# Optimization experiments

Measured on AMD Instinct MI355X. Metric: run time of the kernel, lower is better.

The kernel has to match this reference:

```python
import jax, jax.numpy as jnp
import numpy as np
import math

B, N, DIM, H, DH, NNULL = 2, 2048, 1024, 16, 64, 2
SCALE = 8.0
LN_EPS = 1e-5


def _alibi_slopes(heads):
    # heads is a power of 2 here (16): slopes = start * start**i
    start = 2.0 ** (-(2.0 ** (-(math.log2(heads) - 3))))
    return np.array([start * (start ** i) for i in range(heads)], dtype=np.float32)


def setup_inputs() -> dict:
    key = jax.random.key(0)
    ks = jax.random.split(key, 6)
    inner = H * DH
    return {
        "x": jax.random.normal(ks[0], (B, N, DIM), dtype=jnp.float32),
        "norm_g": jnp.ones((DIM,), jnp.float32),
        "norm_b": jnp.zeros((DIM,), jnp.float32),
        "Wq": jax.random.normal(ks[1], (DIM, inner), jnp.float32) * 0.02,
        "Wkv": jax.random.normal(ks[2], (DIM, 2 * inner), jnp.float32) * 0.02,
        "q_scale": jnp.ones((DH,), jnp.float32),
        "k_scale": jnp.ones((DH,), jnp.float32),
        "null_kv": jax.random.normal(ks[3], (H, 2 * NNULL, DH), jnp.float32),
        "Wout": jax.random.normal(ks[4], (inner, DIM), jnp.float32) * 0.02,
    }


def _l2norm(t):
    # matches F.normalize: x / max(||x||, 1e-12)
    n = jnp.sqrt(jnp.sum(t * t, axis=-1, keepdims=True))
    return t / jnp.maximum(n, 1e-12)


def reference(x, norm_g, norm_b, Wq, Wkv, q_scale, k_scale, null_kv, Wout):
    b, n, dim = x.shape
    h, dh, nn = H, DH, NNULL
    j = n + nn

    # NOTE: faithful to source -- K/V come from the PRE-norm x (kv_input bound
    # before x = self.norm(x)); only Q uses the LayerNorm'd x.
    mu = jnp.mean(x, axis=-1, keepdims=True)
    var = jnp.mean((x - mu) ** 2, axis=-1, keepdims=True)
    xn = (x - mu) * jax.lax.rsqrt(var + LN_EPS) * norm_g + norm_b

    q = (xn @ Wq).reshape(b, n, h, dh).transpose(0, 2, 1, 3)          # b h n d
    kv = x @ Wkv
    k, v = jnp.split(kv, 2, axis=-1)
    k = k.reshape(b, n, h, dh).transpose(0, 2, 1, 3)                   # b h n d
    v = v.reshape(b, n, h, dh).transpose(0, 2, 1, 3)

    # null kv: (h, 2*nn, dh) -> (h, nn, 2, dh)
    null = null_kv.reshape(h, nn, 2, dh)
    nk = jnp.broadcast_to(null[:, :, 0, :][None], (b, h, nn, dh))
    nv = jnp.broadcast_to(null[:, :, 1, :][None], (b, h, nn, dh))
    k = jnp.concatenate([nk, k], axis=2)                               # b h j d
    v = jnp.concatenate([nv, v], axis=2)

    q = _l2norm(q) * q_scale
    k = _l2norm(k) * k_scale

    sim = jnp.einsum('bhid,bhjd->bhij', q, k) * SCALE                  # b h n j

    # ALiBi bias: rows at positions j-n..j-1, cols 0..j-1
    irow = jnp.arange(j - n, j)
    jcol = jnp.arange(j)
    bias = -jnp.abs(jcol[None, :] - irow[:, None]).astype(sim.dtype)   # (n, j)
    slopes = jnp.asarray(_alibi_slopes(h))[:, None, None]              # (h,1,1)
    sim = sim + slopes * bias

    # causal mask: triu with offset j - n + 1 (null kv always visible)
    causal = jnp.triu(jnp.ones((n, j), dtype=bool), k=j - n + 1)
    neg = jnp.finfo(sim.dtype).max
    sim = jnp.where(causal[None, None], -neg, sim)

    attn = jax.nn.softmax(sim, axis=-1)
    out = jnp.einsum('bhij,bhjd->bhid', attn, v)
    out = out.transpose(0, 2, 1, 3).reshape(b, n, h * dh)
    return out @ Wout
```

## Files before the change

### kernel.cpp

```cpp
#include <hip/hip_runtime.h>
#include <stdint.h>

#define H_    16
#define N_    2048
#define DIM_  1024
#define DH_   64
#define NN_   2
#define J_    2050
#define JP_   2112
#define B_    2
#define M_    4096
#define NSEG_ 84

typedef unsigned short u16;
typedef unsigned int u32;
typedef short bf16x8 __attribute__((ext_vector_type(8)));
typedef float f32x4 __attribute__((ext_vector_type(4)));

__device__ __forceinline__ u16 f2b(float f) {
  union { float f; unsigned int i; } v; v.f = f;
  unsigned int r = v.i + 0x7fffu + ((v.i >> 16) & 1u);
  return (u16)(r >> 16);
}
__device__ __forceinline__ float b2f(u16 u) {
  union { unsigned int i; float f; } v; v.i = ((unsigned int)u) << 16; return v.f;
}
__device__ __forceinline__ float lo2f(u32 u) {
  union { u32 i; float f; } v; v.i = u << 16; return v.f;
}
__device__ __forceinline__ float hi2f(u32 u) {
  union { u32 i; float f; } v; v.i = u & 0xffff0000u; return v.f;
}
__device__ __forceinline__ void unp8(const uint4 u, float* d) {
  d[0] = lo2f(u.x); d[1] = hi2f(u.x); d[2] = lo2f(u.y); d[3] = hi2f(u.y);
  d[4] = lo2f(u.z); d[5] = hi2f(u.z); d[6] = lo2f(u.w); d[7] = hi2f(u.w);
}
__device__ __forceinline__ void dma16(const u16* g, u16* l) {
  __builtin_amdgcn_global_load_lds(
      (const __attribute__((address_space(1))) u32*)(const void*)g,
      (__attribute__((address_space(3))) u32*)(void*)l, 16, 0, 0);
}

__global__ __launch_bounds__(256) void ktranspose_cast(const float* __restrict__ in,
                                                       u16* __restrict__ out, int R, int C) {
  __shared__ float tile[32][33];
  int tx = threadIdx.x & 31, ty = threadIdx.x >> 5;
  int c0 = blockIdx.x * 32, r0 = blockIdx.y * 32;
  #pragma unroll
  for (int i = 0; i < 32; i += 8)
    tile[ty + i][tx] = in[(size_t)(r0 + ty + i) * C + c0 + tx];
  __syncthreads();
  #pragma unroll
  for (int i = 0; i < 32; i += 8)
    out[(size_t)(c0 + ty + i) * R + r0 + tx] = f2b(tile[tx][ty + i]);
}

__global__ __launch_bounds__(256) void lnorm_k(const float* __restrict__ x,
                                               const float* __restrict__ g,
                                               const float* __restrict__ bb,
                                               u16* __restrict__ xn,
                                               u16* __restrict__ xbf) {
  int row = blockIdx.x;
  int t = threadIdx.x;
  float4 rw = *(const float4*)(x + (size_t)row * DIM_ + t * 4);
  float v0 = rw.x, v1 = rw.y, v2 = rw.z, v3 = rw.w;
  uint2 cw;
  cw.x = (unsigned)f2b(v0) | ((unsigned)f2b(v1) << 16);
  cw.y = (unsigned)f2b(v2) | ((unsigned)f2b(v3) << 16);
  *(uint2*)(xbf + (size_t)row * DIM_ + t * 4) = cw;
  float s = v0 + v1 + v2 + v3;
  float ss = v0 * v0 + v1 * v1 + v2 * v2 + v3 * v3;
  #pragma unroll
  for (int o = 32; o; o >>= 1) { s += __shfl_xor(s, o, 64); ss += __shfl_xor(ss, o, 64); }
  __shared__ float red[8];
  int lane = t & 63, w = t >> 6;
  if (lane == 0) { red[w] = s; red[4 + w] = ss; }
  __syncthreads();
  float S = red[0] + red[1] + red[2] + red[3];
  float SS = red[4] + red[5] + red[6] + red[7];
  float mu = S * (1.0f / DIM_);
  float var = SS * (1.0f / DIM_) - mu * mu;
  float rs = rsqrtf(var + 1e-5f);
  float4 gv = *(const float4*)(g + t * 4);
  float4 bv = *(const float4*)(bb + t * 4);
  uint2 ow;
  ow.x = (unsigned)f2b((v0 - mu) * rs * gv.x + bv.x) |
         ((unsigned)f2b((v1 - mu) * rs * gv.y + bv.y) << 16);
  ow.y = (unsigned)f2b((v2 - mu) * rs * gv.z + bv.z) |
         ((unsigned)f2b((v3 - mu) * rs * gv.w + bv.w) << 16);
  *(uint2*)(xn + (size_t)row * DIM_ + t * 4) = ow;
}

template <int MODE>
__global__ __launch_bounds__(256, 4) void gemm_k(const u16* __restrict__ A,
                                                 const u16* __restrict__ BT,
                                                 void* __restrict__ dst0,
                                                 void* __restrict__ dst1,
                                                 const float* __restrict__ scale,
                                                 int M, int Nc, int K) {
  __shared__ u16 As[128 * 32];
  __shared__ u16 Bs[64 * 32];
  int tid = threadIdx.x, wv = tid >> 6, lane = tid & 63;
  int fm = lane & 15, fg = lane >> 4;
  int row0 = blockIdx.y * 128, col0 = blockIdx.x * 64;
  f32x4 acc[2][4] = {};
  int lr = lane >> 2, lc8 = (lane & 3) * 8;
  const u16* Ag = A + (size_t)(row0 + wv * 32 + lr) * K + lc8;
  const u16* Bg = BT + (size_t)(col0 + wv * 16 + lr) * K + lc8;
  u16* AsW = As + wv * 1024;
  u16* BsW = Bs + wv * 512;
  for (int k0 = 0; k0 < K; k0 += 32) {
    __syncthreads();
    dma16(Ag + k0, AsW);
    dma16(Ag + (size_t)16 * K + k0, AsW + 512);
    dma16(Bg + k0, BsW);
    __syncthreads();
    bf16x8 af0 = *(const bf16x8*)&As[(wv * 32 + fm) * 32 + fg * 8];
    bf16x8 af1 = *(const bf16x8*)&As[(wv * 32 + 16 + fm) * 32 + fg * 8];
    #pragma unroll
    for (int nt = 0; nt < 4; nt++) {
      bf16x8 bfr = *(const bf16x8*)&Bs[(nt * 16 + fm) * 32 + fg * 8];
      acc[0][nt] = __builtin_amdgcn_mfma_f32_16x16x32_bf16(af0, bfr, acc[0][nt], 0, 0, 0);
      acc[1][nt] = __builtin_amdgcn_mfma_f32_16x16x32_bf16(af1, bfr, acc[1][nt], 0, 0, 0);
    }
  }
  if (MODE == 1) {
    float* C = (float*)dst0;
    #pragma unroll
    for (int mt = 0; mt < 2; mt++)
      #pragma unroll
      for (int nt = 0; nt < 4; nt++)
        #pragma unroll
        for (int r = 0; r < 4; r++) {
          int m = row0 + wv * 32 + mt * 16 + fg * 4 + r;
          C[(size_t)m * Nc + col0 + nt * 16 + fm] = acc[mt][nt][r];
        }
  } else {
    bool isK = (MODE == 2) || (col0 < 1024);
    int h = ((MODE == 2) ? col0 : (isK ? col0 : col0 - 1024)) >> 6;
    float sv[4];
    if (isK) {
      #pragma unroll
      for (int nt = 0; nt < 4; nt++) sv[nt] = scale[nt * 16 + fm];
    }
    u16* Do = (u16*)((MODE == 3 && !isK) ? dst1 : dst0);
    #pragma unroll
    for (int mt = 0; mt < 2; mt++) {
      #pragma unroll
      for (int r = 0; r < 4; r++) {
        float inv = 1.0f;
        if (isK) {
          float ssp = 0.0f;
          #pragma unroll
          for (int nt = 0; nt < 4; nt++) ssp += acc[mt][nt][r] * acc[mt][nt][r];
          #pragma unroll
          for (int o = 1; o <= 8; o <<= 1) ssp += __shfl_xor(ssp, o, 64);
          inv = 1.0f / fmaxf(sqrtf(ssp), 1e-12f);
        }
        int m = row0 + wv * 32 + mt * 16 + fg * 4 + r;
        int b = m >> 11, n = m & 2047;
        size_t base;
        if (MODE == 2)      base = (((size_t)(b * H_ + h)) * N_ + n) * 64;
        else if (isK)       base = (((size_t)(b * H_ + h)) * JP_ + (n + NN_)) * 64;
        else                base = (((size_t)(b * H_ + h)) * J_ + (n + NN_)) * 64;
        #pragma unroll
        for (int nt = 0; nt < 4; nt++) {
          float val = acc[mt][nt][r];
          if (isK) val = val * inv * sv[nt];
          Do[base + nt * 16 + fm] = f2b(val);
        }
      }
    }
  }
}

__global__ __launch_bounds__(256) void vtransp_k(const u16* __restrict__ Vb,
                                                 const float* __restrict__ nkv,
                                                 const float* __restrict__ ks,
                                                 u16* __restrict__ Kb,
                                                 u16* __restrict__ VTp) {
  __shared__ u16 tile[64][80];
  int t = threadIdx.x;
  int c = blockIdx.x, bh = blockIdx.y, h = bh & 15;
  int jl = t >> 2, dc = (t & 3) * 16;
  int j = c * 64 + jl;
  if (j < NN_) {
    float kvv[16];
    float kssp = 0.0f;
    #pragma unroll
    for (int e = 0; e < 16; e++) {
      float vv = nkv[(size_t)(h * 4 + 2 * j + 1) * 64 + dc + e];
      tile[jl][dc + e] = f2b(vv);
      float kv = nkv[(size_t)(h * 4 + 2 * j) * 64 + dc + e];
      kvv[e] = kv; kssp += kv * kv;
    }
    kssp += __shfl_xor(kssp, 1, 64);
    kssp += __shfl_xor(kssp, 2, 64);
    float inv = 1.0f / fmaxf(sqrtf(kssp), 1e-12f);
    #pragma unroll
    for (int e = 0; e < 16; e++)
      Kb[((size_t)bh * JP_ + j) * 64 + dc + e] = f2b(kvv[e] * inv * ks[dc + e]);
  } else if (j < J_) {
    const uint4* src = (const uint4*)(Vb + ((size_t)bh * J_ + j) * 64 + dc);
    *(uint4*)&tile[jl][dc] = src[0];
    *(uint4*)&tile[jl][dc + 8] = src[1];
  } else {
    uint4 z = {0, 0, 0, 0};
    *(uint4*)&tile[jl][dc] = z;
    *(uint4*)&tile[jl][dc + 8] = z;
  }
  __syncthreads();
  int d = t >> 2, p0 = (t & 3) * 16;
  u16 tmp[16] __attribute__((aligned(16)));
  #pragma unroll
  for (int e = 0; e < 16; e++) {
    int pos = p0 + e;
    int h2 = pos >> 5, rem = pos & 31;
    int fgp = rem >> 3, tt = rem & 7;
    int nt = tt >> 2, r = tt & 3;
    int jloc = (h2 * 2 + nt) * 16 + fgp * 4 + r;
    tmp[e] = tile[jloc][d];
  }
  uint4* dstp = (uint4*)(VTp + ((size_t)bh * 64 + d) * JP_ + c * 64 + p0);
  dstp[0] = ((uint4*)tmp)[0];
  dstp[1] = ((uint4*)tmp)[1];
}

__global__ __launch_bounds__(256, 6) void attn_k(const u16* __restrict__ Qn,
                                                 const u16* __restrict__ Kb,
                                                 const u16* __restrict__ VTp,
                                                 const float* __restrict__ qs,
                                                 const float* __restrict__ ks,
                                                 u16* __restrict__ partials) {
  __shared__ u16 Ks0[64 * 32], Ks1[64 * 32];
  __shared__ u16 Vs0[64 * 32], Vs1[64 * 32];
  int tid = threadIdx.x;
  int wv = tid >> 6, lane = tid & 63;
  int fm = lane & 15, fg = lane >> 4;
  int bh = blockIdx.y, h = bh & 15;
  int cum = 0, qt = 0, seg = 0;
  #pragma unroll 1
  for (int i = 0; i < 32; i++) {
    int t = 31 - i, s = (t + 9) >> 3;
    if ((int)blockIdx.x < cum + s) { qt = t; seg = (int)blockIdx.x - cum; break; }
    cum += s;
  }
  int q0 = qt * 64;
  int q = q0 + wv * 16 + fm;
  float slope = exp2f(-0.5f * (float)(h + 1));
  float prod = fabsf(qs[lane] * ks[lane]);
  #pragma unroll
  for (int o = 32; o; o >>= 1) prod = fmaxf(prod, __shfl_xor(prod, o, 64));
  float Mb = 8.0f * prod;
  const u16* qp = Qn + ((size_t)bh * N_ + q) * 64 + fg * 8;
  bf16x8 qf0 = *(const bf16x8*)(qp);
  bf16x8 qf1 = *(const bf16x8*)(qp + 32);
  f32x4 accO[4] = {};
  float lp = 0.0f;
  int lr = lane >> 2, lc8 = (lane & 3) * 8;
  const u16* KbBH = Kb + (size_t)bh * JP_ * 64;
  const u16* VTbh = VTp + (size_t)bh * 64 * JP_;
  int c0 = seg * 8;
  int c1 = min(c0 + 8, qt + 2);
  for (int c = c0; c < c1; c++) {
    int jb = c * 64;
    __syncthreads();
    const u16* Kg = KbBH + (size_t)jb * 64 + (size_t)(wv * 16 + lr) * 64 + lc8;
    dma16(Kg,      Ks0 + wv * 512);
    dma16(Kg + 32, Ks1 + wv * 512);
    const u16* Vg = VTbh + (size_t)(wv * 16 + lr) * JP_ + jb + lc8;
    dma16(Vg,      Vs0 + wv * 512);
    dma16(Vg + 32, Vs1 + wv * 512);
    __syncthreads();
    f32x4 accS[4] = {};
    #pragma unroll
    for (int nt = 0; nt < 4; nt++) {
      bf16x8 kf0 = *(const bf16x8*)&Ks0[(nt * 16 + fm) * 32 + fg * 8];
      accS[nt] = __builtin_amdgcn_mfma_f32_16x16x32_bf16(kf0, qf0, accS[nt], 0, 0, 0);
      bf16x8 kf1 = *(const bf16x8*)&Ks1[(nt * 16 + fm) * 32 + fg * 8];
      accS[nt] = __builtin_amdgcn_mfma_f32_16x16x32_bf16(kf1, qf1, accS[nt], 0, 0, 0);
    }
    union { bf16x8 v; u16 s[8]; } P0, P1;
    #pragma unroll
    for (int nt = 0; nt < 4; nt++) {
      #pragma unroll
      for (int r = 0; r < 4; r++) {
        int jj = jb + nt * 16 + fg * 4 + r;
        float arg = fmaf(accS[nt][r], 8.0f, slope * (float)(jj - q - 2)) - Mb;
        float p = (jj <= q + 2) ? __expf(arg) : 0.0f;
        u16 pb = f2b(p);
        lp += b2f(pb);
        if (nt < 2) P0.s[nt * 4 + r] = pb;
        else        P1.s[(nt - 2) * 4 + r] = pb;
      }
    }
    #pragma unroll
    for (int nt = 0; nt < 4; nt++) {
      bf16x8 vf0 = *(const bf16x8*)&Vs0[(nt * 16 + fm) * 32 + fg * 8];
      accO[nt] = __builtin_amdgcn_mfma_f32_16x16x32_bf16(vf0, P0.v, accO[nt], 0, 0, 0);
      bf16x8 vf1 = *(const bf16x8*)&Vs1[(nt * 16 + fm) * 32 + fg * 8];
      accO[nt] = __builtin_amdgcn_mfma_f32_16x16x32_bf16(vf1, P1.v, accO[nt], 0, 0, 0);
    }
  }
  lp += __shfl_xor(lp, 16, 64);
  lp += __shfl_xor(lp, 32, 64);
  u16* P = partials + ((size_t)bh * NSEG_ + blockIdx.x) * 4224;
  int sq = wv * 16 + fm;
  #pragma unroll
  for (int nt = 0; nt < 4; nt++) {
    uint2 ow;
    ow.x = (unsigned)f2b(accO[nt][0]) | ((unsigned)f2b(accO[nt][1]) << 16);
    ow.y = (unsigned)f2b(accO[nt][2]) | ((unsigned)f2b(accO[nt][3]) << 16);
    *(uint2*)(P + sq * 64 + nt * 16 + fg * 4) = ow;
  }
  if (fg == 0) *(float*)(P + 4096 + 2 * sq) = lp;
}

__global__ __launch_bounds__(256) void comb_k(const u16* __restrict__ partials,
                                              u16* __restrict__ AO) {
  int qt = blockIdx.x, bh = blockIdx.y, b = bh >> 4, h = bh & 15;
  int t = threadIdx.x, q = t >> 2, dq = (t & 3) * 16;
  int s = (qt + 9) >> 3;
  int cum = 0;
  for (int tt = qt + 1; tt < 32; tt++) cum += (tt + 9) >> 3;
  float acc[16] = {};
  float lsum = 0.0f;
  for (int k = 0; k < s; k++) {
    const u16* P = partials + ((size_t)bh * NSEG_ + cum + k) * 4224;
    uint4 a = *(const uint4*)(P + q * 64 + dq);
    uint4 bq = *(const uint4*)(P + q * 64 + dq + 8);
    float tmp[8];
    unp8(a, tmp);
    #pragma unroll
    for (int e = 0; e < 8; e++) acc[e] += tmp[e];
    unp8(bq, tmp);
    #pragma unroll
    for (int e = 0; e < 8; e++) acc[8 + e] += tmp[e];
    lsum += *(const float*)(P + 4096 + 2 * q);
  }
  float linv = 1.0f / lsum;
  int n = qt * 64 + q;
  u16* dst = AO + (((size_t)(b * N_ + n)) * H_ + h) * 64 + dq;
  u16 ov[16] __attribute__((aligned(16)));
  #pragma unroll
  for (int e = 0; e < 16; e++) ov[e] = f2b(acc[e] * linv);
  *(uint4*)dst = ((uint4*)ov)[0];
  *(uint4*)(dst + 8) = ((uint4*)ov)[1];
}

extern "C" void kernel_launch(void* const* d_in, const int* in_sizes, int n_in,
                              void* d_out, int out_size, void* d_ws, size_t ws_size,
                              hipStream_t stream) {
  const float* x    = (const float*)d_in[0];
  const float* ng   = (const float*)d_in[1];
  const float* nb   = (const float*)d_in[2];
  const float* Wq   = (const float*)d_in[3];
  const float* Wkv  = (const float*)d_in[4];
  const float* qs   = (const float*)d_in[5];
  const float* ks   = (const float*)d_in[6];
  const float* nkv  = (const float*)d_in[7];
  const float* Wout = (const float*)d_in[8];
  float* out = (float*)d_out;
  char* ws = (char*)d_ws;

  u16* xn    = (u16*)(ws + 0);
  u16* WoutT = (u16*)(ws + 8388608);
  u16* Qn    = (u16*)(ws + 10485760);
  u16* Kb    = (u16*)(ws + 18874368);
  u16* VTp   = (u16*)(ws + 27525120);
  u16* xbf   = (u16*)(ws + 36175872);
  u16* WqT   = (u16*)(ws + 44564480);
  u16* WkvT  = (u16*)(ws + 46661632);
  u16* Vb    = (u16*)(ws + 50855936);
  u16* parts = xbf;
  u16* AO    = xn;

  hipMemsetAsync(Kb, 0, 8650752, stream);
  ktranspose_cast<<<dim3(32, 32), 256, 0, stream>>>(Wq, WqT, 1024, 1024);
  ktranspose_cast<<<dim3(64, 32), 256, 0, stream>>>(Wkv, WkvT, 1024, 2048);
  ktranspose_cast<<<dim3(32, 32), 256, 0, stream>>>(Wout, WoutT, 1024, 1024);
  lnorm_k<<<4096, 256, 0, stream>>>(x, ng, nb, xn, xbf);
  gemm_k<2><<<dim3(16, 32), 256, 0, stream>>>(xn, WqT, Qn, nullptr, qs, M_, 1024, 1024);
  gemm_k<3><<<dim3(32, 32), 256, 0, stream>>>(xbf, WkvT, Kb, Vb, ks, M_, 2048, 1024);
  vtransp_k<<<dim3(33, 32), 256, 0, stream>>>(Vb, nkv, ks, Kb, VTp);
  attn_k<<<dim3(NSEG_, 32), 256, 0, stream>>>(Qn, Kb, VTp, qs, ks, parts);
  comb_k<<<dim3(32, 32), 256, 0, stream>>>(parts, AO);
  gemm_k<1><<<dim3(16, 32), 256, 0, stream>>>(AO, WoutT, out, nullptr, nullptr, M_, 1024, 1024);
}
```

Measured before the change: 238.8 us.

## Enlarge GEMM tiles to 128x128, fold scale into Q, streamline attention softmax

The GEMM kernel moves from 128x64 to 128x128 block tiles, with each wave computing a 64x64 sub-tile from 4 A and 4 B fragments. This raises MFMA reuse per LDS read and halves the grid. The Q projection now folds the factor of 8 into the q scale. The attention softmax uses precomputed ALiBi offsets, a mask-free fast path for tiles that lie fully below the diagonal, and packed bf16 conversion intrinsics. The larger tile raises register pressure and drops the occupancy hint, and the max-offset term must still agree with the pre-scaled Q.

Result: slower. 286.2 us (+19.9%).

```diff
diff --git a/kernel.cpp b/kernel.cpp
--- a/kernel.cpp
+++ b/kernel.cpp
@@ -1,4 +1,5 @@
 #include <hip/hip_runtime.h>
+#include <hip/hip_bf16.h>
 #include <stdint.h>
 
 #define H_    16
@@ -35,6 +36,11 @@
   d[0] = lo2f(u.x); d[1] = hi2f(u.x); d[2] = lo2f(u.y); d[3] = hi2f(u.y);
   d[4] = lo2f(u.z); d[5] = hi2f(u.z); d[6] = lo2f(u.w); d[7] = hi2f(u.w);
 }
+__device__ __forceinline__ u32 pk2(float a, float b) {
+  union { __hip_bfloat162 h; u32 u; } x;
+  x.h = __float22bfloat162_rn(make_float2(a, b));
+  return x.u;
+}
 __device__ __forceinline__ void dma16(const u16* g, u16* l) {
   __builtin_amdgcn_global_load_lds(
       (const __attribute__((address_space(1))) u32*)(const void*)g,
@@ -65,8 +71,8 @@
   float4 rw = *(const float4*)(x + (size_t)row * DIM_ + t * 4);
   float v0 = rw.x, v1 = rw.y, v2 = rw.z, v3 = rw.w;
   uint2 cw;
-  cw.x = (unsigned)f2b(v0) | ((unsigned)f2b(v1) << 16);
-  cw.y = (unsigned)f2b(v2) | ((unsigned)f2b(v3) << 16);
+  cw.x = pk2(v0, v1);
+  cw.y = pk2(v2, v3);
   *(uint2*)(xbf + (size_t)row * DIM_ + t * 4) = cw;
   float s = v0 + v1 + v2 + v3;
   float ss = v0 * v0 + v1 * v1 + v2 * v2 + v3 * v3;
@@ -84,68 +90,74 @@
   float4 gv = *(const float4*)(g + t * 4);
   float4 bv = *(const float4*)(bb + t * 4);
   uint2 ow;
-  ow.x = (unsigned)f2b((v0 - mu) * rs * gv.x + bv.x) |
-         ((unsigned)f2b((v1 - mu) * rs * gv.y + bv.y) << 16);
-  ow.y = (unsigned)f2b((v2 - mu) * rs * gv.z + bv.z) |
-         ((unsigned)f2b((v3 - mu) * rs * gv.w + bv.w) << 16);
+  ow.x = pk2((v0 - mu) * rs * gv.x + bv.x, (v1 - mu) * rs * gv.y + bv.y);
+  ow.y = pk2((v2 - mu) * rs * gv.z + bv.z, (v3 - mu) * rs * gv.w + bv.w);
   *(uint2*)(xn + (size_t)row * DIM_ + t * 4) = ow;
 }
 
 template <int MODE>
-__global__ __launch_bounds__(256, 4) void gemm_k(const u16* __restrict__ A,
-                                                 const u16* __restrict__ BT,
-                                                 void* __restrict__ dst0,
-                                                 void* __restrict__ dst1,
-                                                 const float* __restrict__ scale,
-                                                 int M, int Nc, int K) {
+__global__ __launch_bounds__(256) void gemm_k(const u16* __restrict__ A,
+                                              const u16* __restrict__ BT,
+                                              void* __restrict__ dst0,
+                                              void* __restrict__ dst1,
+                                              const float* __restrict__ scale,
+                                              int M, int Nc, int K) {
   __shared__ u16 As[128 * 32];
-  __shared__ u16 Bs[64 * 32];
+  __shared__ u16 Bs[128 * 32];
   int tid = threadIdx.x, wv = tid >> 6, lane = tid & 63;
   int fm = lane & 15, fg = lane >> 4;
-  int row0 = blockIdx.y * 128, col0 = blockIdx.x * 64;
-  f32x4 acc[2][4] = {};
+  int row0 = blockIdx.y * 128, col0 = blockIdx.x * 128;
+  int wr = (wv & 1) * 64, wc = (wv >> 1) * 64;
+  f32x4 acc[4][4] = {};
   int lr = lane >> 2, lc8 = (lane & 3) * 8;
   const u16* Ag = A + (size_t)(row0 + wv * 32 + lr) * K + lc8;
-  const u16* Bg = BT + (size_t)(col0 + wv * 16 + lr) * K + lc8;
+  const u16* Bg = BT + (size_t)(col0 + wv * 32 + lr) * K + lc8;
   u16* AsW = As + wv * 1024;
-  u16* BsW = Bs + wv * 512;
+  u16* BsW = Bs + wv * 1024;
   for (int k0 = 0; k0 < K; k0 += 32) {
     __syncthreads();
     dma16(Ag + k0, AsW);
     dma16(Ag + (size_t)16 * K + k0, AsW + 512);
     dma16(Bg + k0, BsW);
+    dma16(Bg + (size_t)16 * K + k0, BsW + 512);
     __syncthreads();
-    bf16x8 af0 = *(const bf16x8*)&As[(wv * 32 + fm) * 32 + fg * 8];
-    bf16x8 af1 = *(const bf16x8*)&As[(wv * 32 + 16 + fm) * 32 + fg * 8];
-    #pragma unroll
-    for (int nt = 0; nt < 4; nt++) {
-      bf16x8 bfr = *(const bf16x8*)&Bs[(nt * 16 + fm) * 32 + fg * 8];
-      acc[0][nt] = __builtin_amdgcn_mfma_f32_16x16x32_bf16(af0, bfr, acc[0][nt], 0, 0, 0);
-      acc[1][nt] = __builtin_amdgcn_mfma_f32_16x16x32_bf16(af1, bfr, acc[1][nt], 0, 0, 0);
-    }
+    bf16x8 af[4], bfv[4];
+    #pragma unroll
+    for (int mt = 0; mt < 4; mt++)
+      af[mt] = *(const bf16x8*)&As[(wr + mt * 16 + fm) * 32 + fg * 8];
+    #pragma unroll
+    for (int nt = 0; nt < 4; nt++)
+      bfv[nt] = *(const bf16x8*)&Bs[(wc + nt * 16 + fm) * 32 + fg * 8];
+    #pragma unroll
+    for (int mt = 0; mt < 4; mt++)
+      #pragma unroll
+      for (int nt = 0; nt < 4; nt++)
+        acc[mt][nt] = __builtin_amdgcn_mfma_f32_16x16x32_bf16(af[mt], bfv[nt], acc[mt][nt], 0, 0, 0);
   }
   if (MODE == 1) {
     float* C = (float*)dst0;
     #pragma unroll
-    for (int mt = 0; mt < 2; mt++)
-      #pragma unroll
-      for (int nt = 0; nt < 4; nt++)
+    for (int mt = 0; mt < 4; mt++)
+      #pragma unroll
+      for (int r = 0; r < 4; r++) {
+        int m = row0 + wr + mt * 16 + fg * 4 + r;
         #pragma unroll
-        for (int r = 0; r < 4; r++) {
-          int m = row0 + wv * 32 + mt * 16 + fg * 4 + r;
-          C[(size_t)m * Nc + col0 + nt * 16 + fm] = acc[mt][nt][r];
-        }
+        for (int nt = 0; nt < 4; nt++)
+          C[(size_t)m * Nc + col0 + wc + nt * 16 + fm] = acc[mt][nt][r];
+      }
   } else {
-    bool isK = (MODE == 2) || (col0 < 1024);
-    int h = ((MODE == 2) ? col0 : (isK ? col0 : col0 - 1024)) >> 6;
+    int cb = col0 + wc;
+    bool isK = (MODE == 2) || (cb < 1024);
+    int h = (isK ? cb : cb - 1024) >> 6;
     float sv[4];
     if (isK) {
-      #pragma unroll
-      for (int nt = 0; nt < 4; nt++) sv[nt] = scale[nt * 16 + fm];
+      float mul = (MODE == 2) ? 8.0f : 1.0f;
+      #pragma unroll
+      for (int nt = 0; nt < 4; nt++) sv[nt] = scale[nt * 16 + fm] * mul;
     }
     u16* Do = (u16*)((MODE == 3 && !isK) ? dst1 : dst0);
     #pragma unroll
-    for (int mt = 0; mt < 2; mt++) {
+    for (int mt = 0; mt < 4; mt++) {
       #pragma unroll
       for (int r = 0; r < 4; r++) {
         float inv = 1.0f;
@@ -157,7 +169,7 @@
           for (int o = 1; o <= 8; o <<= 1) ssp += __shfl_xor(ssp, o, 64);
           inv = 1.0f / fmaxf(sqrtf(ssp), 1e-12f);
         }
-        int m = row0 + wv * 32 + mt * 16 + fg * 4 + r;
+        int m = row0 + wr + mt * 16 + fg * 4 + r;
         int b = m >> 11, n = m & 2047;
         size_t base;
         if (MODE == 2)      base = (((size_t)(b * H_ + h)) * N_ + n) * 64;
@@ -252,6 +264,12 @@
   #pragma unroll
   for (int o = 32; o; o >>= 1) prod = fmaxf(prod, __shfl_xor(prod, o, 64));
   float Mb = 8.0f * prod;
+  float boff[4][4];
+  #pragma unroll
+  for (int nt = 0; nt < 4; nt++)
+    #pragma unroll
+    for (int r = 0; r < 4; r++)
+      boff[nt][r] = slope * (float)(nt * 16 + fg * 4 + r);
   const u16* qp = Qn + ((size_t)bh * N_ + q) * 64 + fg * 8;
   bf16x8 qf0 = *(const bf16x8*)(qp);
   bf16x8 qf1 = *(const bf16x8*)(qp + 32);
@@ -280,20 +298,39 @@
       bf16x8 kf1 = *(const bf16x8*)&Ks1[(nt * 16 + fm) * 32 + fg * 8];
       accS[nt] = __builtin_amdgcn_mfma_f32_16x16x32_bf16(kf1, qf1, accS[nt], 0, 0, 0);
     }
-    union { bf16x8 v; u16 s[8]; } P0, P1;
-    #pragma unroll
-    for (int nt = 0; nt < 4; nt++) {
-      #pragma unroll
-      for (int r = 0; r < 4; r++) {
-        int jj = jb + nt * 16 + fg * 4 + r;
-        float arg = fmaf(accS[nt][r], 8.0f, slope * (float)(jj - q - 2)) - Mb;
-        float p = (jj <= q + 2) ? __expf(arg) : 0.0f;
-        u16 pb = f2b(p);
-        lp += b2f(pb);
-        if (nt < 2) P0.s[nt * 4 + r] = pb;
-        else        P1.s[(nt - 2) * 4 + r] = pb;
+    float bias0 = slope * (float)(jb - q - 2) - Mb;
+    bool full = (jb + 61 <= q0 + wv * 16);
+    union { bf16x8 v; u32 u[4]; } P0, P1;
+    float lt = 0.0f;
+    if (full) {
+      #pragma unroll
+      for (int nt = 0; nt < 4; nt++) {
+        float p[4];
+        #pragma unroll
+        for (int r = 0; r < 4; r++)
+          p[r] = __expf((accS[nt][r] + boff[nt][r]) + bias0);
+        lt += (p[0] + p[1]) + (p[2] + p[3]);
+        u32 w0 = pk2(p[0], p[1]), w1 = pk2(p[2], p[3]);
+        if (nt < 2) { P0.u[nt * 2] = w0; P0.u[nt * 2 + 1] = w1; }
+        else        { P1.u[(nt - 2) * 2] = w0; P1.u[(nt - 2) * 2 + 1] = w1; }
       }
-    }
+    } else {
+      int lim = q + 2 - jb;
+      #pragma unroll
+      for (int nt = 0; nt < 4; nt++) {
+        float p[4];
+        #pragma unroll
+        for (int r = 0; r < 4; r++) {
+          float a_ = (accS[nt][r] + boff[nt][r]) + bias0;
+          p[r] = (nt * 16 + fg * 4 + r <= lim) ? __expf(a_) : 0.0f;
+        }
+        lt += (p[0] + p[1]) + (p[2] + p[3]);
+        u32 w0 = pk2(p[0], p[1]), w1 = pk2(p[2], p[3]);
+        if (nt < 2) { P0.u[nt * 2] = w0; P0.u[nt * 2 + 1] = w1; }
+        else        { P1.u[(nt - 2) * 2] = w0; P1.u[(nt - 2) * 2 + 1] = w1; }
+      }
+    }
+    lp += lt;
     #pragma unroll
     for (int nt = 0; nt < 4; nt++) {
       bf16x8 vf0 = *(const bf16x8*)&Vs0[(nt * 16 + fm) * 32 + fg * 8];
@@ -309,8 +346,8 @@
   #pragma unroll
   for (int nt = 0; nt < 4; nt++) {
     uint2 ow;
-    ow.x = (unsigned)f2b(accO[nt][0]) | ((unsigned)f2b(accO[nt][1]) << 16);
-    ow.y = (unsigned)f2b(accO[nt][2]) | ((unsigned)f2b(accO[nt][3]) << 16);
+    ow.x = pk2(accO[nt][0], accO[nt][1]);
+    ow.y = pk2(accO[nt][2], accO[nt][3]);
     *(uint2*)(P + sq * 64 + nt * 16 + fg * 4) = ow;
   }
   if (fg == 0) *(float*)(P + 4096 + 2 * sq) = lp;
@@ -380,10 +417,10 @@
   ktranspose_cast<<<dim3(64, 32), 256, 0, stream>>>(Wkv, WkvT, 1024, 2048);
   ktranspose_cast<<<dim3(32, 32), 256, 0, stream>>>(Wout, WoutT, 1024, 1024);
   lnorm_k<<<4096, 256, 0, stream>>>(x, ng, nb, xn, xbf);
-  gemm_k<2><<<dim3(16, 32), 256, 0, stream>>>(xn, WqT, Qn, nullptr, qs, M_, 1024, 1024);
-  gemm_k<3><<<dim3(32, 32), 256, 0, stream>>>(xbf, WkvT, Kb, Vb, ks, M_, 2048, 1024);
+  gemm_k<2><<<dim3(8, 32), 256, 0, stream>>>(xn, WqT, Qn, nullptr, qs, M_, 1024, 1024);
+  gemm_k<3><<<dim3(16, 32), 256, 0, stream>>>(xbf, WkvT, Kb, Vb, ks, M_, 2048, 1024);
   vtransp_k<<<dim3(33, 32), 256, 0, stream>>>(Vb, nkv, ks, Kb, VTp);
   attn_k<<<dim3(NSEG_, 32), 256, 0, stream>>>(Qn, Kb, VTp, qs, ks, parts);
   comb_k<<<dim3(32, 32), 256, 0, stream>>>(parts, AO);
-  gemm_k<1><<<dim3(16, 32), 256, 0, stream>>>(AO, WoutT, out, nullptr, nullptr, M_, 1024, 1024);
-}
+  gemm_k<1><<<dim3(8, 32), 256, 0, stream>>>(AO, WoutT, out, nullptr, nullptr, M_, 1024, 1024);
+}
```
